# Kernel tuning notes

Measured on AMD Instinct MI355X. Metric: run time of the kernel, lower is better.

## Reference

```python
import jax, jax.numpy as jnp
import numpy as np

B, S, E = 2, 2048, 1024
H, KV, D = 16, 4, 64
GC = 128          # ve_gate_channels
EPS = 1.1920929e-07  # torch F.rms_norm default eps for fp32
NEG = -1e30


def setup_inputs() -> dict:
    key = jax.random.key(0)
    ks = jax.random.split(key, 8)
    x = jax.random.normal(ks[0], (B, S, E), jnp.float32)
    ve = jax.random.normal(ks[1], (B, S, KV * D), jnp.float32)
    half = D // 2
    inv_freq = 1.0 / (10000.0 ** (np.arange(half, dtype=np.float64) / half))
    ang = np.arange(S, dtype=np.float64)[:, None] * inv_freq[None, :]
    cos = jnp.asarray(np.cos(ang), jnp.float32)[:, None, :]  # [S,1,D/2]
    sin = jnp.asarray(np.sin(ang), jnp.float32)[:, None, :]
    sc = E ** -0.5
    Wq = jax.random.normal(ks[2], (E, H * D), jnp.float32) * sc
    Wk = jax.random.normal(ks[3], (E, KV * D), jnp.float32) * sc
    Wv = jax.random.normal(ks[4], (E, KV * D), jnp.float32) * sc
    Wproj = jax.random.normal(ks[5], (E, E), jnp.float32) * sc
    Wgate = jax.random.normal(ks[6], (GC, KV), jnp.float32) * (GC ** -0.5)
    return {"x": x, "ve": ve, "cos": cos, "sin": sin, "Wq": Wq, "Wk": Wk,
            "Wv": Wv, "Wproj": Wproj, "Wgate": Wgate,
            "window_left": 1024, "window_right": 0}


def _rms(x):
    return x * jax.lax.rsqrt(jnp.mean(x * x, axis=-1, keepdims=True) + EPS)


def _rope(x, cos, sin):
    d = x.shape[-1] // 2
    x1, x2 = x[..., :d], x[..., d:]
    return jnp.concatenate([x1 * cos + x2 * sin, -x1 * sin + x2 * cos], axis=-1)


def reference(x, ve, cos, sin, Wq, Wk, Wv, Wproj, Wgate, window_left, window_right):
    b, s, e = x.shape
    q = (x @ Wq).reshape(b, s, H, D)
    k = (x @ Wk).reshape(b, s, KV, D)
    v = (x @ Wv).reshape(b, s, KV, D)
    # value-embedding gate: 2*sigmoid over first GC channels, per kv-head
    gate = 2.0 * jax.nn.sigmoid(x[..., :GC] @ Wgate)          # [B,S,KV]
    v = v + gate[..., None] * ve.reshape(b, s, KV, D)
    q = _rms(_rope(q, cos, sin))
    k = _rms(_rope(k, cos, sin))
    # GQA: repeat kv heads to match query heads
    g = H // KV
    kk = jnp.repeat(k, g, axis=2)                             # [B,S,H,D]
    vv = jnp.repeat(v, g, axis=2)
    scores = jnp.einsum('bihd,bjhd->bhij', q, kk) * (D ** -0.5)
    i = jnp.arange(s)[:, None]
    j = jnp.arange(s)[None, :]
    mask = (j <= i + window_right) & (j >= i - window_left) & (j <= i)
    scores = jnp.where(mask, scores, NEG)
    p = jax.nn.softmax(scores, axis=-1)
    y = jnp.einsum('bhij,bjhd->bihd', p, vv).reshape(b, s, H * D)
    return y @ Wproj
```

## Files before the change

kernel.cpp:

```cpp
#include <hip/hip_runtime.h>

typedef __bf16 bf16;
typedef __bf16 bf16x4 __attribute__((ext_vector_type(4)));
typedef __bf16 bf16x8 __attribute__((ext_vector_type(8)));
typedef float floatx4 __attribute__((ext_vector_type(4)));

#define EPS 1.1920929e-07f
#define QSCALE (0.125f * 1.44269504088896f)
#define SHIFT_C 11.5416f

__device__ __forceinline__ floatx4 mfma16(bf16x8 a, bf16x8 b, floatx4 c) {
  return __builtin_amdgcn_mfma_f32_16x16x32_bf16(a, b, c, 0, 0, 0);
}

__device__ __forceinline__ void gload16(const void* g, void* l) {
  __builtin_amdgcn_global_load_lds((const __attribute__((address_space(1))) unsigned int*)g,
                                   (__attribute__((address_space(3))) unsigned int*)l, 16, 0, 0);
}

__global__ void prep_kernel(const float* __restrict__ x, const float* __restrict__ wgate,
                            const float* __restrict__ Wq, const float* __restrict__ Wk,
                            const float* __restrict__ Wv, const float* __restrict__ Wproj,
                            bf16* __restrict__ xb, float* __restrict__ gate,
                            bf16* __restrict__ out_qkv, bf16* __restrict__ out_proj) {
  __shared__ float tile[32][33];
  const int tid = threadIdx.x;
  if (blockIdx.x < 4096) {
    int t = blockIdx.x;
    const float* xr = x + (size_t)t * 1024;
    float4 v = *(const float4*)(xr + tid * 4);
    bf16x4 o = {(bf16)v.x, (bf16)v.y, (bf16)v.z, (bf16)v.w};
    *(bf16x4*)(xb + (size_t)t * 1024 + tid * 4) = o;
    if (tid < 64) {
      int c = (tid & 31) * 4;
#pragma unroll
      for (int kv = 0; kv < 4; kv++) {
        float g = v.x * wgate[(c + 0) * 4 + kv] + v.y * wgate[(c + 1) * 4 + kv] +
                  v.z * wgate[(c + 2) * 4 + kv] + v.w * wgate[(c + 3) * 4 + kv];
        g += __shfl_xor(g, 1, 64);
        g += __shfl_xor(g, 2, 64);
        g += __shfl_xor(g, 4, 64);
        g += __shfl_xor(g, 8, 64);
        g += __shfl_xor(g, 16, 64);
        if (tid == 0) {
          int b = t >> 11, s = t & 2047;
          gate[((size_t)b * 4 + kv) * 2048 + s] = 2.f / (1.f + __expf(-g));
        }
      }
    }
  } else {
    int j = blockIdx.x - 4096;
    int ky = j / 80;
    int nx = j - ky * 80;
    int k0 = ky * 32;
    int tx = tid & 31, ty = tid >> 5;
    if (nx < 48) {
      int n0 = nx * 32;
#pragma unroll
      for (int i = 0; i < 4; i++) {
        int k = k0 + ty + i * 8, n = n0 + tx;
        float v;
        if (n < 1024)      v = Wq[(size_t)k * 1024 + n];
        else if (n < 1280) v = Wk[(size_t)k * 256 + (n - 1024)];
        else               v = Wv[(size_t)k * 256 + (n - 1280)];
        tile[ty + i * 8][tx] = v;
      }
      __syncthreads();
#pragma unroll
      for (int i = 0; i < 4; i++) {
        int n = n0 + ty + i * 8, k = k0 + tx;
        out_qkv[(size_t)n * 1024 + k] = (bf16)tile[tx][ty + i * 8];
      }
    } else {
      int n0 = (nx - 48) * 32;
#pragma unroll
      for (int i = 0; i < 4; i++)
        tile[ty + i * 8][tx] = Wproj[(size_t)(k0 + ty + i * 8) * 1024 + n0 + tx];
      __syncthreads();
#pragma unroll
      for (int i = 0; i < 4; i++)
        out_proj[(size_t)(n0 + ty + i * 8) * 1024 + k0 + tx] = (bf16)tile[tx][ty + i * 8];
    }
  }
}

__global__ __launch_bounds__(256) void qkv_gemm_kernel(const bf16* __restrict__ A,
                                                       const bf16* __restrict__ Bt,
                                                       const float* __restrict__ ve,
                                                       const float* __restrict__ cosb,
                                                       const float* __restrict__ sinb,
                                                       const float* __restrict__ gate,
                                                       bf16* __restrict__ Qb,
                                                       bf16* __restrict__ Kf,
                                                       bf16* __restrict__ Vf) {
  __shared__ __align__(16) char smem[24576];
  bf16* As = (bf16*)smem;
  bf16* Bs = (bf16*)(smem + 16384);
  bf16* Ep = (bf16*)smem;
  const int K = 1024;
  const int tid = threadIdx.x;
  const int orig = blockIdx.x;
  const int lid = (orig & 7) * 96 + (orig >> 3);
  const int tile = lid % 24;
  const int m0 = (lid / 24) * 128, n0 = tile * 64;
  const int w = tid >> 6, lane = tid & 63;
  const int q = lane >> 4, r0 = lane & 15;
  const int lrow = lane >> 2, lcol = (lane & 3) * 8;
  const int b = m0 >> 11, s0 = m0 & 2047;

  floatx4 acc[2][4];
#pragma unroll
  for (int i = 0; i < 2; i++)
#pragma unroll
    for (int j = 0; j < 4; j++) acc[i][j] = (floatx4){0.f, 0.f, 0.f, 0.f};

  for (int k0 = 0; k0 < K; k0 += 64) {
    __syncthreads();
#pragma unroll
    for (int i = 0; i < 4; i++) {
      int g = w * 4 + i, s = g >> 3, rb = g & 7;
      gload16(A + (size_t)(m0 + rb * 16 + lrow) * K + k0 + s * 32 + lcol, &As[s * 4096 + rb * 512]);
    }
#pragma unroll
    for (int i = 0; i < 2; i++) {
      int g = w * 2 + i, s = g >> 2, rb = g & 3;
      gload16(Bt + (size_t)(n0 + rb * 16 + lrow) * K + k0 + s * 32 + lcol, &Bs[s * 2048 + rb * 512]);
    }
    __syncthreads();
#pragma unroll
    for (int s = 0; s < 2; s++) {
      bf16x8 af[2], bfr[4];
#pragma unroll
      for (int mt = 0; mt < 2; mt++) af[mt] = *(const bf16x8*)&As[s * 4096 + (w * 32 + mt * 16 + r0) * 32 + q * 8];
#pragma unroll
      for (int nt = 0; nt < 4; nt++) bfr[nt] = *(const bf16x8*)&Bs[s * 2048 + (nt * 16 + r0) * 32 + q * 8];
#pragma unroll
      for (int mt = 0; mt < 2; mt++)
#pragma unroll
        for (int nt = 0; nt < 4; nt++)
          acc[mt][nt] = mfma16(af[mt], bfr[nt], acc[mt][nt]);
    }
  }
  __syncthreads();

  if (tile < 16) {
    const int h = tile;
#pragma unroll
    for (int mt = 0; mt < 2; mt++) {
      float rvv[4][4];
#pragma unroll
      for (int ntp = 0; ntp < 2; ntp++) {
        int d31 = ntp * 16 + r0;
#pragma unroll
        for (int r = 0; r < 4; r++) {
          int s = s0 + w * 32 + mt * 16 + q * 4 + r;
          float c = cosb[s * 32 + d31], sn = sinb[s * 32 + d31];
          float v1 = acc[mt][ntp][r], v2 = acc[mt][ntp + 2][r];
          rvv[ntp][r] = v1 * c + v2 * sn;
          rvv[ntp + 2][r] = v2 * c - v1 * sn;
        }
      }
#pragma unroll
      for (int r = 0; r < 4; r++) {
        float ss = 0.f;
#pragma unroll
        for (int nt = 0; nt < 4; nt++) ss += rvv[nt][r] * rvv[nt][r];
        ss += __shfl_xor(ss, 1, 64);
        ss += __shfl_xor(ss, 2, 64);
        ss += __shfl_xor(ss, 4, 64);
        ss += __shfl_xor(ss, 8, 64);
        float sc = rsqrtf(ss * (1.f / 64.f) + EPS) * QSCALE;
        int row = w * 32 + mt * 16 + q * 4 + r;
#pragma unroll
        for (int nt = 0; nt < 4; nt++)
          Ep[row * 72 + nt * 16 + r0] = (bf16)(rvv[nt][r] * sc);
      }
    }
    __syncthreads();
#pragma unroll
    for (int p = 0; p < 4; p++) {
      int g = p * 256 + tid;
      int row = g >> 3, chunk = g & 7;
      *(uint4*)&Qb[(((size_t)b * 16 + h) * 2048 + s0 + row) * 64 + chunk * 8] =
          *(const uint4*)&Ep[row * 72 + chunk * 8];
    }
  } else if (tile < 20) {
    const int kv = tile - 16;
#pragma unroll
    for (int mt = 0; mt < 2; mt++) {
      float rvv[4][4];
#pragma unroll
      for (int ntp = 0; ntp < 2; ntp++) {
        int d31 = ntp * 16 + r0;
#pragma unroll
        for (int r = 0; r < 4; r++) {
          int s = s0 + w * 32 + mt * 16 + q * 4 + r;
          float c = cosb[s * 32 + d31], sn = sinb[s * 32 + d31];
          float v1 = acc[mt][ntp][r], v2 = acc[mt][ntp + 2][r];
          rvv[ntp][r] = v1 * c + v2 * sn;
          rvv[ntp + 2][r] = v2 * c - v1 * sn;
        }
      }
#pragma unroll
      for (int r = 0; r < 4; r++) {
        float ss = 0.f;
#pragma unroll
        for (int nt = 0; nt < 4; nt++) ss += rvv[nt][r] * rvv[nt][r];
        ss += __shfl_xor(ss, 1, 64);
        ss += __shfl_xor(ss, 2, 64);
        ss += __shfl_xor(ss, 4, 64);
        ss += __shfl_xor(ss, 8, 64);
        float sc = rsqrtf(ss * (1.f / 64.f) + EPS);
        int row = w * 32 + mt * 16 + q * 4 + r;
#pragma unroll
        for (int nt = 0; nt < 4; nt++)
          Ep[row * 72 + nt * 16 + r0] = (bf16)(rvv[nt][r] * sc);
      }
    }
    __syncthreads();
    {
      int tk = (s0 >> 5) + w;
      size_t tb = ((size_t)(b * 4 + kv) * 64 + tk) * 2048;
#pragma unroll
      for (int u = 0; u < 4; u++) {
        int joff = (u >= 2) ? 16 : 0, doff = (u & 1) * 32;
        bf16x8 f = *(const bf16x8*)&Ep[(w * 32 + joff + r0) * 72 + doff + q * 8];
        *(bf16x8*)&Kf[tb + u * 512 + lane * 8] = f;
      }
    }
  } else {
    const int kv = tile - 20;
    const float* gbase = gate + ((size_t)b * 4 + kv) * 2048;
#pragma unroll
    for (int mt = 0; mt < 2; mt++) {
#pragma unroll
      for (int r = 0; r < 4; r++) {
        int row = w * 32 + mt * 16 + q * 4 + r;
        float gg = gbase[s0 + row];
#pragma unroll
        for (int nt = 0; nt < 4; nt++) {
          int d = nt * 16 + r0;
          float vv = acc[mt][nt][r] + gg * ve[(size_t)(m0 + row) * 256 + kv * 64 + d];
          Ep[row * 72 + d] = (bf16)vv;
        }
      }
    }
    __syncthreads();
    {
      int tk = (s0 >> 5) + w;
      size_t tb = ((size_t)(b * 4 + kv) * 64 + tk) * 2048;
#pragma unroll
      for (int nt = 0; nt < 4; nt++) {
        bf16 tmp[8];
#pragma unroll
        for (int e = 0; e < 8; e++) {
          int jl = w * 32 + (e >> 2) * 16 + 4 * q + (e & 3);
          tmp[e] = Ep[jl * 72 + nt * 16 + r0];
        }
        *(uint4*)&Vf[tb + nt * 512 + lane * 8] = *(uint4*)tmp;
      }
    }
  }
}

__global__ __launch_bounds__(256) void proj_gemm_kernel(const bf16* __restrict__ A,
                                                        const bf16* __restrict__ Bt,
                                                        float* __restrict__ Cout) {
  __shared__ __align__(16) bf16 As[2 * 128 * 32];
  __shared__ __align__(16) bf16 Bs[2 * 64 * 32];
  const int K = 1024, N = 1024;
  const int tid = threadIdx.x;
  const int orig = blockIdx.x;
  const int lid = (orig & 7) * 64 + (orig >> 3);
  const int m0 = (lid / 16) * 128, n0 = (lid % 16) * 64;
  const int w = tid >> 6, lane = tid & 63;
  const int q = lane >> 4, r0 = lane & 15;
  const int lrow = lane >> 2, lcol = (lane & 3) * 8;

  floatx4 acc[2][4];
#pragma unroll
  for (int i = 0; i < 2; i++)
#pragma unroll
    for (int j = 0; j < 4; j++) acc[i][j] = (floatx4){0.f, 0.f, 0.f, 0.f};

  for (int k0 = 0; k0 < K; k0 += 64) {
    __syncthreads();
#pragma unroll
    for (int i = 0; i < 4; i++) {
      int g = w * 4 + i, s = g >> 3, rb = g & 7;
      gload16(A + (size_t)(m0 + rb * 16 + lrow) * K + k0 + s * 32 + lcol, &As[s * 4096 + rb * 512]);
    }
#pragma unroll
    for (int i = 0; i < 2; i++) {
      int g = w * 2 + i, s = g >> 2, rb = g & 3;
      gload16(Bt + (size_t)(n0 + rb * 16 + lrow) * K + k0 + s * 32 + lcol, &Bs[s * 2048 + rb * 512]);
    }
    __syncthreads();
#pragma unroll
    for (int s = 0; s < 2; s++) {
      bf16x8 af[2], bfr[4];
#pragma unroll
      for (int mt = 0; mt < 2; mt++) af[mt] = *(const bf16x8*)&As[s * 4096 + (w * 32 + mt * 16 + r0) * 32 + q * 8];
#pragma unroll
      for (int nt = 0; nt < 4; nt++) bfr[nt] = *(const bf16x8*)&Bs[s * 2048 + (nt * 16 + r0) * 32 + q * 8];
#pragma unroll
      for (int mt = 0; mt < 2; mt++)
#pragma unroll
        for (int nt = 0; nt < 4; nt++)
          acc[mt][nt] = mfma16(af[mt], bfr[nt], acc[mt][nt]);
    }
  }
#pragma unroll
  for (int mt = 0; mt < 2; mt++)
#pragma unroll
    for (int nt = 0; nt < 4; nt++)
#pragma unroll
      for (int r = 0; r < 4; r++) {
        int row = m0 + w * 32 + mt * 16 + q * 4 + r;
        int col = n0 + nt * 16 + r0;
        Cout[(size_t)row * N + col] = acc[mt][nt][r];
      }
}

__global__ __launch_bounds__(256, 4) void attn_kernel(const bf16* __restrict__ Qb,
                                                      const bf16* __restrict__ Kf,
                                                      const bf16* __restrict__ Vf,
                                                      const int* __restrict__ wlp,
                                                      const int* __restrict__ wrp,
                                                      bf16* __restrict__ Yb) {
  __shared__ __align__(16) bf16 Ks[4 * 2048];
  __shared__ __align__(16) bf16 Vs[4 * 2048];
  const int wl = wlp[0];
  const int wrc = min(wrp[0], 0);
  const int blk = blockIdx.x;
  const int bkv = blk & 7;
  const int b = bkv >> 2, kvh = bkv & 3;
  const int cm = 127 - (blk >> 3);
  const int w = threadIdx.x >> 6, lane = threadIdx.x & 63;
  const int q = lane >> 4, r0 = lane & 15;
  const int h = kvh * 4 + w;
  const int q0 = cm << 4;

  const bf16* qbase = Qb + (((size_t)b * 16 + h) * 2048 + q0 + r0) * 64;
  bf16x8 aq0 = *(const bf16x8*)(qbase + q * 8);
  bf16x8 aq1 = *(const bf16x8*)(qbase + 32 + q * 8);

  floatx4 O[4];
#pragma unroll
  for (int nt = 0; nt < 4; nt++) O[nt] = (floatx4){0.f, 0.f, 0.f, 0.f};
  floatx4 L = (floatx4){0.f, 0.f, 0.f, 0.f};

  const bf16 onev = (bf16)1.0f;
  const bf16x8 ones = {onev, onev, onev, onev, onev, onev, onev, onev};

  const int jlo = max(0, q0 - wl) & ~31;
  const int jhi = q0 + 15 + wrc;
  const int count = ((jhi - jlo) >> 5) + 1;
  const int tile0 = jlo >> 5;

  const bf16* kfb = Kf + ((size_t)(b * 4 + kvh) * 64) * 2048;
  const bf16* vfb = Vf + ((size_t)(b * 4 + kvh) * 64) * 2048;

  for (int t = 0; t < count;) {
    const int ns = min(4, count - t);
    __syncthreads();
    for (int c = w; c < ns * 8; c += 4) {
      int u = c >> 3, rem = c & 7;
      if (rem < 4)
        gload16(kfb + (size_t)(tile0 + t + u) * 2048 + rem * 512 + lane * 8,
                &Ks[u * 2048 + rem * 512]);
      else
        gload16(vfb + (size_t)(tile0 + t + u) * 2048 + (rem - 4) * 512 + lane * 8,
                &Vs[u * 2048 + (rem - 4) * 512]);
    }
    __syncthreads();

    for (int u = 0; u < ns; u++) {
      const int j0 = jlo + ((t + u) << 5);
      const bf16* Ku = &Ks[u * 2048];
      const bf16* Vu = &Vs[u * 2048];

      bf16x8 kf0 = *(const bf16x8*)&Ku[0 * 512 + lane * 8];
      bf16x8 kf1 = *(const bf16x8*)&Ku[1 * 512 + lane * 8];
      bf16x8 kf2 = *(const bf16x8*)&Ku[2 * 512 + lane * 8];
      bf16x8 kf3 = *(const bf16x8*)&Ku[3 * 512 + lane * 8];

      floatx4 s0 = (floatx4){-SHIFT_C, -SHIFT_C, -SHIFT_C, -SHIFT_C};
      floatx4 s1 = s0;
      __builtin_amdgcn_s_setprio(1);
      s0 = mfma16(kf0, aq0, s0);
      s0 = mfma16(kf1, aq1, s0);
      s1 = mfma16(kf2, aq0, s1);
      s1 = mfma16(kf3, aq1, s1);
      __builtin_amdgcn_s_setprio(0);

      bf16x8 pa;
      if (j0 >= q0 + 15 - wl && j0 + 31 <= q0 + wrc) {
#pragma unroll
        for (int r = 0; r < 4; r++) {
          pa[r] = (bf16)exp2f(s0[r]);
          pa[4 + r] = (bf16)exp2f(s1[r]);
        }
      } else {
        const int i = q0 + r0;
#pragma unroll
        for (int r = 0; r < 4; r++) {
          int ja = j0 + 4 * q + r, jb = ja + 16;
          bool va = (ja <= i + wrc) && (ja >= i - wl);
          bool vb = (jb <= i + wrc) && (jb >= i - wl);
          pa[r] = va ? (bf16)exp2f(s0[r]) : (bf16)0.f;
          pa[4 + r] = vb ? (bf16)exp2f(s1[r]) : (bf16)0.f;
        }
      }

      bf16x8 vf0 = *(const bf16x8*)&Vu[0 * 512 + lane * 8];
      bf16x8 vf1 = *(const bf16x8*)&Vu[1 * 512 + lane * 8];
      bf16x8 vf2 = *(const bf16x8*)&Vu[2 * 512 + lane * 8];
      bf16x8 vf3 = *(const bf16x8*)&Vu[3 * 512 + lane * 8];

      __builtin_amdgcn_s_setprio(1);
      L = mfma16(pa, ones, L);
      O[0] = mfma16(pa, vf0, O[0]);
      O[1] = mfma16(pa, vf1, O[1]);
      O[2] = mfma16(pa, vf2, O[2]);
      O[3] = mfma16(pa, vf3, O[3]);
      __builtin_amdgcn_s_setprio(0);
    }
    t += ns;
  }

  float inv[4];
#pragma unroll
  for (int r = 0; r < 4; r++) inv[r] = 1.f / L[r];
#pragma unroll
  for (int nt = 0; nt < 4; nt++)
#pragma unroll
    for (int r = 0; r < 4; r++) {
      int i = q0 + q * 4 + r;
      Yb[((size_t)b * 2048 + i) * 1024 + h * 64 + nt * 16 + r0] = (bf16)(O[nt][r] * inv[r]);
    }
}

extern "C" void kernel_launch(void* const* d_in, const int* in_sizes, int n_in,
                              void* d_out, int out_size, void* d_ws, size_t ws_size,
                              hipStream_t stream) {
  const float* x     = (const float*)d_in[0];
  const float* ve    = (const float*)d_in[1];
  const float* cosb  = (const float*)d_in[2];
  const float* sinb  = (const float*)d_in[3];
  const float* Wq    = (const float*)d_in[4];
  const float* Wk    = (const float*)d_in[5];
  const float* Wv    = (const float*)d_in[6];
  const float* Wproj = (const float*)d_in[7];
  const float* Wgate = (const float*)d_in[8];
  const int* wl      = (const int*)d_in[9];
  const int* wr      = (const int*)d_in[10];

  char* ws = (char*)d_ws;
  bf16* Xb      = (bf16*)(ws);
  bf16* Wqkv_t  = (bf16*)(ws + 8388608);
  bf16* Wproj_t = (bf16*)(ws + 11534336);
  bf16* Qb      = (bf16*)(ws + 13631488);
  bf16* Kf      = (bf16*)(ws + 22020096);
  bf16* Vf      = (bf16*)(ws + 24117248);
  bf16* Yb      = (bf16*)(ws + 26214400);
  float* gateb  = (float*)(ws + 34603008);

  prep_kernel<<<4096 + 2560, 256, 0, stream>>>(x, Wgate, Wq, Wk, Wv, Wproj, Xb, gateb, Wqkv_t, Wproj_t);
  qkv_gemm_kernel<<<768, 256, 0, stream>>>(Xb, Wqkv_t, ve, cosb, sinb, gateb, Qb, Kf, Vf);
  attn_kernel<<<1024, 256, 0, stream>>>(Qb, Kf, Vf, wl, wr, Yb);
  proj_gemm_kernel<<<512, 256, 0, stream>>>(Yb, Wproj_t, (float*)d_out);
}
```

Before: 167.1 us.

## Double-buffer K/V tiles via register prefetch in attention kernel

Replaces the batched 4-tile global_load_lds staging with a two-slot LDS double buffer. Each iteration prefetches the next 32-key K/V tile into registers with plain global loads while computing on the current slot, then stores it to the other slot. The aim is to hide global load latency behind the MFMA work. The cost is two barriers per tile instead of two per four tiles, extra VGPRs for the prefetch, and a redundant reload of the last tile.

```diff
diff --git a/kernel.cpp b/kernel.cpp
--- a/kernel.cpp
+++ b/kernel.cpp
@@ -328,15 +328,16 @@
                                                       const int* __restrict__ wlp,
                                                       const int* __restrict__ wrp,
                                                       bf16* __restrict__ Yb) {
-  __shared__ __align__(16) bf16 Ks[4 * 2048];
-  __shared__ __align__(16) bf16 Vs[4 * 2048];
+  __shared__ __align__(16) bf16 Ks[2][2048];
+  __shared__ __align__(16) bf16 Vs[2][2048];
+  const int tid = threadIdx.x;
   const int wl = wlp[0];
   const int wrc = min(wrp[0], 0);
   const int blk = blockIdx.x;
   const int bkv = blk & 7;
   const int b = bkv >> 2, kvh = bkv & 3;
   const int cm = 127 - (blk >> 3);
-  const int w = threadIdx.x >> 6, lane = threadIdx.x & 63;
+  const int w = tid >> 6, lane = tid & 63;
   const int q = lane >> 4, r0 = lane & 15;
   const int h = kvh * 4 + w;
   const int q0 = cm << 4;
@@ -361,72 +362,74 @@
   const bf16* kfb = Kf + ((size_t)(b * 4 + kvh) * 64) * 2048;
   const bf16* vfb = Vf + ((size_t)(b * 4 + kvh) * 64) * 2048;
 
-  for (int t = 0; t < count;) {
-    const int ns = min(4, count - t);
-    __syncthreads();
-    for (int c = w; c < ns * 8; c += 4) {
-      int u = c >> 3, rem = c & 7;
-      if (rem < 4)
-        gload16(kfb + (size_t)(tile0 + t + u) * 2048 + rem * 512 + lane * 8,
-                &Ks[u * 2048 + rem * 512]);
-      else
-        gload16(vfb + (size_t)(tile0 + t + u) * 2048 + (rem - 4) * 512 + lane * 8,
-                &Vs[u * 2048 + (rem - 4) * 512]);
-    }
-    __syncthreads();
-
-    for (int u = 0; u < ns; u++) {
-      const int j0 = jlo + ((t + u) << 5);
-      const bf16* Ku = &Ks[u * 2048];
-      const bf16* Vu = &Vs[u * 2048];
-
-      bf16x8 kf0 = *(const bf16x8*)&Ku[0 * 512 + lane * 8];
-      bf16x8 kf1 = *(const bf16x8*)&Ku[1 * 512 + lane * 8];
-      bf16x8 kf2 = *(const bf16x8*)&Ku[2 * 512 + lane * 8];
-      bf16x8 kf3 = *(const bf16x8*)&Ku[3 * 512 + lane * 8];
-
-      floatx4 s0 = (floatx4){-SHIFT_C, -SHIFT_C, -SHIFT_C, -SHIFT_C};
-      floatx4 s1 = s0;
-      __builtin_amdgcn_s_setprio(1);
-      s0 = mfma16(kf0, aq0, s0);
-      s0 = mfma16(kf1, aq1, s0);
-      s1 = mfma16(kf2, aq0, s1);
-      s1 = mfma16(kf3, aq1, s1);
-      __builtin_amdgcn_s_setprio(0);
-
-      bf16x8 pa;
-      if (j0 >= q0 + 15 - wl && j0 + 31 <= q0 + wrc) {
-#pragma unroll
-        for (int r = 0; r < 4; r++) {
-          pa[r] = (bf16)exp2f(s0[r]);
-          pa[4 + r] = (bf16)exp2f(s1[r]);
-        }
-      } else {
-        const int i = q0 + r0;
-#pragma unroll
-        for (int r = 0; r < 4; r++) {
-          int ja = j0 + 4 * q + r, jb = ja + 16;
-          bool va = (ja <= i + wrc) && (ja >= i - wl);
-          bool vb = (jb <= i + wrc) && (jb >= i - wl);
-          pa[r] = va ? (bf16)exp2f(s0[r]) : (bf16)0.f;
-          pa[4 + r] = vb ? (bf16)exp2f(s1[r]) : (bf16)0.f;
-        }
-      }
-
-      bf16x8 vf0 = *(const bf16x8*)&Vu[0 * 512 + lane * 8];
-      bf16x8 vf1 = *(const bf16x8*)&Vu[1 * 512 + lane * 8];
-      bf16x8 vf2 = *(const bf16x8*)&Vu[2 * 512 + lane * 8];
-      bf16x8 vf3 = *(const bf16x8*)&Vu[3 * 512 + lane * 8];
-
-      __builtin_amdgcn_s_setprio(1);
-      L = mfma16(pa, ones, L);
-      O[0] = mfma16(pa, vf0, O[0]);
-      O[1] = mfma16(pa, vf1, O[1]);
-      O[2] = mfma16(pa, vf2, O[2]);
-      O[3] = mfma16(pa, vf3, O[3]);
-      __builtin_amdgcn_s_setprio(0);
-    }
-    t += ns;
+  {
+    uint4 kr = *(const uint4*)(kfb + (size_t)tile0 * 2048 + tid * 8);
+    uint4 vr = *(const uint4*)(vfb + (size_t)tile0 * 2048 + tid * 8);
+    *(uint4*)&Ks[0][tid * 8] = kr;
+    *(uint4*)&Vs[0][tid * 8] = vr;
+  }
+  __syncthreads();
+
+  int cur = 0;
+  for (int t = 0; t < count; t++) {
+    const int j0 = jlo + (t << 5);
+    const int tn = (t + 1 < count) ? tile0 + t + 1 : tile0 + t;
+    uint4 kr = *(const uint4*)(kfb + (size_t)tn * 2048 + tid * 8);
+    uint4 vr = *(const uint4*)(vfb + (size_t)tn * 2048 + tid * 8);
+
+    const bf16* Ku = &Ks[cur][0];
+    const bf16* Vu = &Vs[cur][0];
+    bf16x8 kf0 = *(const bf16x8*)&Ku[0 * 512 + lane * 8];
+    bf16x8 kf1 = *(const bf16x8*)&Ku[1 * 512 + lane * 8];
+    bf16x8 kf2 = *(const bf16x8*)&Ku[2 * 512 + lane * 8];
+    bf16x8 kf3 = *(const bf16x8*)&Ku[3 * 512 + lane * 8];
+
+    floatx4 s0 = (floatx4){-SHIFT_C, -SHIFT_C, -SHIFT_C, -SHIFT_C};
+    floatx4 s1 = s0;
+    __builtin_amdgcn_s_setprio(1);
+    s0 = mfma16(kf0, aq0, s0);
+    s0 = mfma16(kf1, aq1, s0);
+    s1 = mfma16(kf2, aq0, s1);
+    s1 = mfma16(kf3, aq1, s1);
+    __builtin_amdgcn_s_setprio(0);
+
+    bf16x8 pa;
+    if (j0 >= q0 + 15 - wl && j0 + 31 <= q0 + wrc) {
+#pragma unroll
+      for (int r = 0; r < 4; r++) {
+        pa[r] = (bf16)exp2f(s0[r]);
+        pa[4 + r] = (bf16)exp2f(s1[r]);
+      }
+    } else {
+      const int i = q0 + r0;
+#pragma unroll
+      for (int r = 0; r < 4; r++) {
+        int ja = j0 + 4 * q + r, jb = ja + 16;
+        bool va = (ja <= i + wrc) && (ja >= i - wl);
+        bool vb = (jb <= i + wrc) && (jb >= i - wl);
+        pa[r] = va ? (bf16)exp2f(s0[r]) : (bf16)0.f;
+        pa[4 + r] = vb ? (bf16)exp2f(s1[r]) : (bf16)0.f;
+      }
+    }
+
+    bf16x8 vf0 = *(const bf16x8*)&Vu[0 * 512 + lane * 8];
+    bf16x8 vf1 = *(const bf16x8*)&Vu[1 * 512 + lane * 8];
+    bf16x8 vf2 = *(const bf16x8*)&Vu[2 * 512 + lane * 8];
+    bf16x8 vf3 = *(const bf16x8*)&Vu[3 * 512 + lane * 8];
+
+    __builtin_amdgcn_s_setprio(1);
+    L = mfma16(pa, ones, L);
+    O[0] = mfma16(pa, vf0, O[0]);
+    O[1] = mfma16(pa, vf1, O[1]);
+    O[2] = mfma16(pa, vf2, O[2]);
+    O[3] = mfma16(pa, vf3, O[3]);
+    __builtin_amdgcn_s_setprio(0);
+
+    __syncthreads();
+    *(uint4*)&Ks[cur ^ 1][tid * 8] = kr;
+    *(uint4*)&Vs[cur ^ 1][tid * 8] = vr;
+    __syncthreads();
+    cur ^= 1;
   }
 
   float inv[4];
```

New measurement: 160.0 us (median of 2 runs). 1.04x faster.
